# Kernel optimization log

Hardware: AMD Instinct MI355X
Metric: run time of the kernel (lower is better)

## Reference

```python
import jax, jax.numpy as jnp
import numpy as np
import math

B, C, H, W = 8, 64, 64, 64

def setup_inputs() -> dict:
    key = jax.random.key(0)
    k1, k2 = jax.random.split(key)
    x1 = jax.random.normal(k1, (B, C, H, W), dtype=jnp.float32)
    x2 = jax.random.normal(k2, (B, C, H, W), dtype=jnp.float32)
    return {"x1": x1, "x2": x2}

def reference(x1, x2):
    b, c, h, w = x1.shape
    # flatten spatial dims -> tokens: [B, HW, C]
    x1f = x1.reshape(b, c, h * w).transpose(0, 2, 1)
    x2f = x2.reshape(b, c, h * w).transpose(0, 2, 1)
    scale = 1.0 / math.sqrt(c)
    # direction A: queries from x1, keys/values from x2
    scores_a = jnp.einsum('bqc,bkc->bqk', x1f, x2f) * scale  # [B, HW, HW]
    out_a = jnp.einsum('bqk,bkc->bqc', jax.nn.softmax(scores_a, axis=-1), x2f)
    # direction B: queries from x2, keys/values from x1
    scores_b = jnp.einsum('bqc,bkc->bqk', x2f, x1f) * scale
    out_b = jnp.einsum('bqk,bkc->bqc', jax.nn.softmax(scores_b, axis=-1), x1f)
    out = (out_a + out_b).transpose(0, 2, 1).reshape(b, c, h, w)
    return out
```

## Files before the change

kernel.cpp:

```cpp
#include <hip/hip_runtime.h>
#include <hip/hip_bf16.h>
#include <stdint.h>


#define TT 4096
#define CC 64
#define NB 8

typedef float f32x4 __attribute__((ext_vector_type(4)));
typedef float f32x4a __attribute__((ext_vector_type(4), may_alias));
typedef short s16x8 __attribute__((ext_vector_type(8)));
typedef unsigned int u32x2a __attribute__((ext_vector_type(2), may_alias));
typedef unsigned int u32x4a __attribute__((ext_vector_type(4), may_alias));
typedef float f32a __attribute__((may_alias));

static __device__ __forceinline__ unsigned fbits(float x) { return __float_as_uint(x); }
static __device__ __forceinline__ ushort bf16of(float v) {
    return (ushort)((fbits(v) + 0x8000u) >> 16);
}
static __device__ __forceinline__ unsigned pack2(float a, float b) {
    return __builtin_amdgcn_perm(fbits(b) + 0x8000u, fbits(a) + 0x8000u, 0x07060302u);
}
static __device__ __forceinline__ s16x8 load_frag(const void* p) {
    u32x4a t = *(const u32x4a*)p;
    return __builtin_bit_cast(s16x8, t);
}

#define SQC1 0.4246609177f

__global__ void prep_k(const float* __restrict__ x1, const float* __restrict__ x2,
                       ushort* __restrict__ kt, ushort* __restrict__ vt) {
    const int inp = blockIdx.z, b = blockIdx.y, tt = blockIdx.x;
    const float* src = (inp == 0 ? x1 : x2) + (size_t)b * CC * TT;
    const size_t plane = (size_t)TT * CC;
    ushort* kd = kt + (size_t)(inp * NB + b) * plane;
    ushort* vd = vt + (size_t)(inp * NB + b) * plane;
    __shared__ ushort lds[64][72];
    const int tid = threadIdx.x;
    const int c  = tid >> 2;
    const int tg = tid & 3;
    const float* srow = src + (size_t)c * TT + tt * 64 + tg * 16;
    unsigned hw[8];
#pragma unroll
    for (int i = 0; i < 4; ++i) {
        f32x4a v = *(const f32x4a*)(srow + i * 4);
        hw[2 * i]     = pack2(v[0], v[1]);
        hw[2 * i + 1] = pack2(v[2], v[3]);
#pragma unroll
        for (int k = 0; k < 4; ++k) lds[tg * 16 + i * 4 + k][c] = bf16of(v[k] * SQC1);
    }
    {
        ushort* vchunk = vd + (((size_t)tt * 2 + (tg >> 1)) * 4 + (c >> 4)) * 512;
        const int l16v = c & 15;
        const int q0v  = (tg & 1) * 2;
        u32x4a w0 = {hw[0], hw[1], hw[2], hw[3]};
        u32x4a w1 = {hw[4], hw[5], hw[6], hw[7]};
        *(u32x4a*)(vchunk + (size_t)(q0v * 16 + l16v) * 8)       = w0;
        *(u32x4a*)(vchunk + (size_t)((q0v + 1) * 16 + l16v) * 8) = w1;
    }
    __syncthreads();
    const int mt   = tid >> 6;
    const int quad = (tid >> 4) & 3;
    const int l16  = tid & 15;
    const int t    = mt * 16 + l16;
#pragma unroll
    for (int ch = 0; ch < 2; ++ch) {
        u32x4a w = *(const u32x4a*)&lds[t][ch * 32 + quad * 8];
        *(u32x4a*)(kd + (((size_t)tt * 4 + mt) * 2 + ch) * 512 +
                   (size_t)(quad * 16 + l16) * 8) = w;
    }
}

__global__ __attribute__((amdgpu_flat_work_group_size(512, 512)))
void attn_fused_k(const ushort* __restrict__ kt, const ushort* __restrict__ vt,
                  float* __restrict__ out) {
    const int b    = blockIdx.x & 7;
    const int qt   = blockIdx.x >> 3;
    const int tid  = threadIdx.x;
    const int wave = tid >> 6;
    const int lane = tid & 63;
    const int quad = lane >> 4;
    const int l16  = lane & 15;
    const int dir  = wave & 1;
    const int pair = (wave >> 1) & 1;
    const int ks   = wave >> 2;
    const int q0   = qt * 64 + pair * 32;

    const size_t plane = (size_t)TT * CC;
    const ushort* Qp = kt + (size_t)((dir == 0 ? 0 : NB) + b) * plane + (size_t)lane * 8;
    const ushort* Kp = kt + (size_t)((dir == 0 ? NB : 0) + b) * plane + (size_t)lane * 8;
    const ushort* Vp = vt + (size_t)((dir == 0 ? NB : 0) + b) * plane + (size_t)lane * 8;

    __shared__ __align__(16) ushort pbuf[8][2][2][16][72];
    __shared__ float lpx[8][2][16];
    f32a* xbuf = (f32a*)&pbuf[0][0][0][0][0];

    s16x8 qf[2][2];
#pragma unroll
    for (int rb = 0; rb < 2; ++rb)
#pragma unroll
        for (int ch = 0; ch < 2; ++ch)
            qf[rb][ch] = load_frag(Qp + (((size_t)qt * 4 + pair * 2 + rb) * 2 + ch) * 512);

    f32x4 accO[2][4];
#pragma unroll
    for (int rb = 0; rb < 2; ++rb)
#pragma unroll
        for (int ct = 0; ct < 4; ++ct) accO[rb][ct] = (f32x4){0.f, 0.f, 0.f, 0.f};
    float lp[2] = {0.f, 0.f};

    s16x8 kA0, kA1, kA2, kA3, kA4, kA5, kA6, kA7;
    s16x8 kB0, kB1, kB2, kB3, kB4, kB5, kB6, kB7;
    s16x8 vA0, vA1, vA2, vA3, vA4, vA5, vA6, vA7;
    s16x8 vB0, vB1, vB2, vB3, vB4, vB5, vB6, vB7;

    auto loadKA = [&](int j) {
        const ushort* p = Kp + (size_t)(ks * 32 + j) * 4096;
        kA0 = load_frag(p);          kA1 = load_frag(p + 512);
        kA2 = load_frag(p + 1024);   kA3 = load_frag(p + 1536);
        kA4 = load_frag(p + 2048);   kA5 = load_frag(p + 2560);
        kA6 = load_frag(p + 3072);   kA7 = load_frag(p + 3584);
    };
    auto loadKB = [&](int j) {
        const ushort* p = Kp + (size_t)(ks * 32 + j) * 4096;
        kB0 = load_frag(p);          kB1 = load_frag(p + 512);
        kB2 = load_frag(p + 1024);   kB3 = load_frag(p + 1536);
        kB4 = load_frag(p + 2048);   kB5 = load_frag(p + 2560);
        kB6 = load_frag(p + 3072);   kB7 = load_frag(p + 3584);
    };
    auto loadVA = [&](int j) {
        const ushort* p = Vp + (size_t)(ks * 32 + j) * 4096;
        vA0 = load_frag(p);          vA1 = load_frag(p + 512);
        vA2 = load_frag(p + 1024);   vA3 = load_frag(p + 1536);
        vA4 = load_frag(p + 2048);   vA5 = load_frag(p + 2560);
        vA6 = load_frag(p + 3072);   vA7 = load_frag(p + 3584);
    };
    auto loadVB = [&](int j) {
        const ushort* p = Vp + (size_t)(ks * 32 + j) * 4096;
        vB0 = load_frag(p);          vB1 = load_frag(p + 512);
        vB2 = load_frag(p + 1024);   vB3 = load_frag(p + 1536);
        vB4 = load_frag(p + 2048);   vB5 = load_frag(p + 2560);
        vB6 = load_frag(p + 3072);   vB7 = load_frag(p + 3584);
    };

    auto SmT = [&](s16x8 kc0, s16x8 kc1, int mt, int par) {
#pragma unroll
        for (int rb = 0; rb < 2; ++rb) {
            f32x4 s = (f32x4){0.f, 0.f, 0.f, 0.f};
            s = __builtin_amdgcn_mfma_f32_16x16x32_bf16(kc0, qf[rb][0], s, 0, 0, 0);
            s = __builtin_amdgcn_mfma_f32_16x16x32_bf16(kc1, qf[rb][1], s, 0, 0, 0);
            float p0 = __builtin_amdgcn_exp2f(s[0]);
            float p1 = __builtin_amdgcn_exp2f(s[1]);
            float p2 = __builtin_amdgcn_exp2f(s[2]);
            float p3 = __builtin_amdgcn_exp2f(s[3]);
            lp[rb] += (p0 + p1) + (p2 + p3);
            u32x2a w;
            w[0] = pack2(p0, p1);
            w[1] = pack2(p2, p3);
            *(u32x2a*)&pbuf[wave][par][rb][l16][mt * 16 + quad * 4] = w;
        }
    };
    auto PVA = [&]() {
        s16x8 pf0a = load_frag(&pbuf[wave][0][0][l16][quad * 8]);
        s16x8 pf1a = load_frag(&pbuf[wave][0][1][l16][quad * 8]);
        accO[0][0] = __builtin_amdgcn_mfma_f32_16x16x32_bf16(vA0, pf0a, accO[0][0], 0, 0, 0);
        accO[1][0] = __builtin_amdgcn_mfma_f32_16x16x32_bf16(vA0, pf1a, accO[1][0], 0, 0, 0);
        accO[0][1] = __builtin_amdgcn_mfma_f32_16x16x32_bf16(vA1, pf0a, accO[0][1], 0, 0, 0);
        accO[1][1] = __builtin_amdgcn_mfma_f32_16x16x32_bf16(vA1, pf1a, accO[1][1], 0, 0, 0);
        accO[0][2] = __builtin_amdgcn_mfma_f32_16x16x32_bf16(vA2, pf0a, accO[0][2], 0, 0, 0);
        accO[1][2] = __builtin_amdgcn_mfma_f32_16x16x32_bf16(vA2, pf1a, accO[1][2], 0, 0, 0);
        accO[0][3] = __builtin_amdgcn_mfma_f32_16x16x32_bf16(vA3, pf0a, accO[0][3], 0, 0, 0);
        accO[1][3] = __builtin_amdgcn_mfma_f32_16x16x32_bf16(vA3, pf1a, accO[1][3], 0, 0, 0);
        s16x8 pf0b = load_frag(&pbuf[wave][0][0][l16][32 + quad * 8]);
        s16x8 pf1b = load_frag(&pbuf[wave][0][1][l16][32 + quad * 8]);
        accO[0][0] = __builtin_amdgcn_mfma_f32_16x16x32_bf16(vA4, pf0b, accO[0][0], 0, 0, 0);
        accO[1][0] = __builtin_amdgcn_mfma_f32_16x16x32_bf16(vA4, pf1b, accO[1][0], 0, 0, 0);
        accO[0][1] = __builtin_amdgcn_mfma_f32_16x16x32_bf16(vA5, pf0b, accO[0][1], 0, 0, 0);
        accO[1][1] = __builtin_amdgcn_mfma_f32_16x16x32_bf16(vA5, pf1b, accO[1][1], 0, 0, 0);
        accO[0][2] = __builtin_amdgcn_mfma_f32_16x16x32_bf16(vA6, pf0b, accO[0][2], 0, 0, 0);
        accO[1][2] = __builtin_amdgcn_mfma_f32_16x16x32_bf16(vA6, pf1b, accO[1][2], 0, 0, 0);
        accO[0][3] = __builtin_amdgcn_mfma_f32_16x16x32_bf16(vA7, pf0b, accO[0][3], 0, 0, 0);
        accO[1][3] = __builtin_amdgcn_mfma_f32_16x16x32_bf16(vA7, pf1b, accO[1][3], 0, 0, 0);
    };
    auto PVB = [&]() {
        s16x8 pf0a = load_frag(&pbuf[wave][1][0][l16][quad * 8]);
        s16x8 pf1a = load_frag(&pbuf[wave][1][1][l16][quad * 8]);
        accO[0][0] = __builtin_amdgcn_mfma_f32_16x16x32_bf16(vB0, pf0a, accO[0][0], 0, 0, 0);
        accO[1][0] = __builtin_amdgcn_mfma_f32_16x16x32_bf16(vB0, pf1a, accO[1][0], 0, 0, 0);
        accO[0][1] = __builtin_amdgcn_mfma_f32_16x16x32_bf16(vB1, pf0a, accO[0][1], 0, 0, 0);
        accO[1][1] = __builtin_amdgcn_mfma_f32_16x16x32_bf16(vB1, pf1a, accO[1][1], 0, 0, 0);
        accO[0][2] = __builtin_amdgcn_mfma_f32_16x16x32_bf16(vB2, pf0a, accO[0][2], 0, 0, 0);
        accO[1][2] = __builtin_amdgcn_mfma_f32_16x16x32_bf16(vB2, pf1a, accO[1][2], 0, 0, 0);
        accO[0][3] = __builtin_amdgcn_mfma_f32_16x16x32_bf16(vB3, pf0a, accO[0][3], 0, 0, 0);
        accO[1][3] = __builtin_amdgcn_mfma_f32_16x16x32_bf16(vB3, pf1a, accO[1][3], 0, 0, 0);
        s16x8 pf0b = load_frag(&pbuf[wave][1][0][l16][32 + quad * 8]);
        s16x8 pf1b = load_frag(&pbuf[wave][1][1][l16][32 + quad * 8]);
        accO[0][0] = __builtin_amdgcn_mfma_f32_16x16x32_bf16(vB4, pf0b, accO[0][0], 0, 0, 0);
        accO[1][0] = __builtin_amdgcn_mfma_f32_16x16x32_bf16(vB4, pf1b, accO[1][0], 0, 0, 0);
        accO[0][1] = __builtin_amdgcn_mfma_f32_16x16x32_bf16(vB5, pf0b, accO[0][1], 0, 0, 0);
        accO[1][1] = __builtin_amdgcn_mfma_f32_16x16x32_bf16(vB5, pf1b, accO[1][1], 0, 0, 0);
        accO[0][2] = __builtin_amdgcn_mfma_f32_16x16x32_bf16(vB6, pf0b, accO[0][2], 0, 0, 0);
        accO[1][2] = __builtin_amdgcn_mfma_f32_16x16x32_bf16(vB6, pf1b, accO[1][2], 0, 0, 0);
        accO[0][3] = __builtin_amdgcn_mfma_f32_16x16x32_bf16(vB7, pf0b, accO[0][3], 0, 0, 0);
        accO[1][3] = __builtin_amdgcn_mfma_f32_16x16x32_bf16(vB7, pf1b, accO[1][3], 0, 0, 0);
    };

    loadKA(0);
    loadVA(0);
#pragma unroll 1
    for (int j = 0; j < 32; j += 2) {
        loadKB(j + 1);
        SmT(kA0, kA1, 0, 0); SmT(kA2, kA3, 1, 0); SmT(kA4, kA5, 2, 0); SmT(kA6, kA7, 3, 0);
        loadVB(j + 1);
        SmT(kB0, kB1, 0, 1); SmT(kB2, kB3, 1, 1); SmT(kB4, kB5, 2, 1); SmT(kB6, kB7, 3, 1);
        if (j + 2 < 32) loadKA(j + 2);
        PVA();
        if (j + 2 < 32) loadVA(j + 2);
        PVB();
    }

    float inv[2];
#pragma unroll
    for (int rb = 0; rb < 2; ++rb) {
        float l = lp[rb];
        l += __shfl_xor(l, 16);
        l += __shfl_xor(l, 32);
        lp[rb] = l;
        if (lane < 16) lpx[wave][rb][l16] = l;
    }
    __syncthreads();
#pragma unroll
    for (int rb = 0; rb < 2; ++rb)
        inv[rb] = __builtin_amdgcn_rcpf(lp[rb] + lpx[wave ^ 4][rb][l16]);

    const int g = (ks << 1) | dir;
#pragma unroll 1
    for (int ph = 3; ph >= 1; --ph) {
        if (g == ph) {
#pragma unroll
            for (int rb = 0; rb < 2; ++rb)
#pragma unroll
                for (int ct = 0; ct < 4; ++ct)
#pragma unroll
                    for (int r = 0; r < 4; ++r) {
                        const int slot = (pair * 32 + rb * 16 + ct * 4 + r) * 64 + lane;
                        float v = accO[rb][ct][r] * inv[rb];
                        if (ph == 3) xbuf[slot] = v;
                        else xbuf[slot] += v;
                    }
        }
        __syncthreads();
    }
    if (g == 0) {
        float* ob = out + (size_t)b * plane;
#pragma unroll
        for (int rb = 0; rb < 2; ++rb)
#pragma unroll
            for (int ct = 0; ct < 4; ++ct)
#pragma unroll
                for (int r = 0; r < 4; ++r) {
                    float v = accO[rb][ct][r] * inv[rb] +
                              xbuf[(pair * 32 + rb * 16 + ct * 4 + r) * 64 + lane];
                    ob[(size_t)(ct * 16 + quad * 4 + r) * TT + q0 + rb * 16 + l16] = v;
                }
    }
}

extern "C" void kernel_launch(void* const* d_in, const int* in_sizes, int n_in,
                              void* d_out, int out_size, void* d_ws, size_t ws_size,
                              hipStream_t stream) {
    const float* x1 = (const float*)d_in[0];
    const float* x2 = (const float*)d_in[1];
    ushort* kt = (ushort*)d_ws;
    ushort* vt = (ushort*)d_ws + (size_t)2 * NB * TT * CC;

    hipLaunchKernelGGL(prep_k, dim3(TT / 64, NB, 2), dim3(256), 0, stream, x1, x2, kt, vt);
    hipLaunchKernelGGL(attn_fused_k, dim3(64 * NB), dim3(512), 0, stream,
                       kt, vt, (float*)d_out);
}
```

Before: 163.6 us.

## Use 1024-thread blocks covering two query tiles with single-buffered K/V fragments

The attention kernel now runs 16 waves per block, with each block handling two 64-query tiles, so the grid is halved and the shared pbuf/lpx arrays are doubled. The separate A/B register buffers for K and V fragments are merged into one set. The main loop is re-pipelined so the PV step for one parity overlaps with the score step and loads for the other. The goal is to cut register pressure enough to fit 1024-thread blocks and raise the number of resident waves. In exchange there is less register-level prefetch depth, more LDS per block, and a tighter per-wave register budget that could cause spills.

```diff
diff --git a/kernel.cpp b/kernel.cpp
--- a/kernel.cpp
+++ b/kernel.cpp
@@ -71,28 +71,30 @@
     }
 }
 
-__global__ __attribute__((amdgpu_flat_work_group_size(512, 512)))
+__global__ __attribute__((amdgpu_flat_work_group_size(1024, 1024)))
 void attn_fused_k(const ushort* __restrict__ kt, const ushort* __restrict__ vt,
                   float* __restrict__ out) {
-    const int b    = blockIdx.x & 7;
-    const int qt   = blockIdx.x >> 3;
-    const int tid  = threadIdx.x;
-    const int wave = tid >> 6;
-    const int lane = tid & 63;
-    const int quad = lane >> 4;
-    const int l16  = lane & 15;
-    const int dir  = wave & 1;
-    const int pair = (wave >> 1) & 1;
-    const int ks   = wave >> 2;
-    const int q0   = qt * 64 + pair * 32;
+    const int b     = blockIdx.x & 7;
+    const int qt2   = blockIdx.x >> 3;
+    const int tid   = threadIdx.x;
+    const int wave  = tid >> 6;
+    const int lane  = tid & 63;
+    const int quad  = lane >> 4;
+    const int l16   = lane & 15;
+    const int dir   = wave & 1;
+    const int pair  = (wave >> 1) & 1;
+    const int ks    = (wave >> 2) & 1;
+    const int qsub  = wave >> 3;
+    const int qt    = qt2 * 2 + qsub;
+    const int q0    = qt * 64 + pair * 32;
 
     const size_t plane = (size_t)TT * CC;
     const ushort* Qp = kt + (size_t)((dir == 0 ? 0 : NB) + b) * plane + (size_t)lane * 8;
     const ushort* Kp = kt + (size_t)((dir == 0 ? NB : 0) + b) * plane + (size_t)lane * 8;
     const ushort* Vp = vt + (size_t)((dir == 0 ? NB : 0) + b) * plane + (size_t)lane * 8;
 
-    __shared__ __align__(16) ushort pbuf[8][2][2][16][72];
-    __shared__ float lpx[8][2][16];
+    __shared__ __align__(16) ushort pbuf[16][2][2][16][72];
+    __shared__ float lpx[16][2][16];
     f32a* xbuf = (f32a*)&pbuf[0][0][0][0][0];
 
     s16x8 qf[2][2];
@@ -110,40 +112,29 @@
     float lp[2] = {0.f, 0.f};
 
     s16x8 kA0, kA1, kA2, kA3, kA4, kA5, kA6, kA7;
-    s16x8 kB0, kB1, kB2, kB3, kB4, kB5, kB6, kB7;
     s16x8 vA0, vA1, vA2, vA3, vA4, vA5, vA6, vA7;
-    s16x8 vB0, vB1, vB2, vB3, vB4, vB5, vB6, vB7;
-
-    auto loadKA = [&](int j) {
+
+    auto loadK = [&](int j) {
         const ushort* p = Kp + (size_t)(ks * 32 + j) * 4096;
         kA0 = load_frag(p);          kA1 = load_frag(p + 512);
         kA2 = load_frag(p + 1024);   kA3 = load_frag(p + 1536);
         kA4 = load_frag(p + 2048);   kA5 = load_frag(p + 2560);
         kA6 = load_frag(p + 3072);   kA7 = load_frag(p + 3584);
     };
-    auto loadKB = [&](int j) {
-        const ushort* p = Kp + (size_t)(ks * 32 + j) * 4096;
-        kB0 = load_frag(p);          kB1 = load_frag(p + 512);
-        kB2 = load_frag(p + 1024);   kB3 = load_frag(p + 1536);
-        kB4 = load_frag(p + 2048);   kB5 = load_frag(p + 2560);
-        kB6 = load_frag(p + 3072);   kB7 = load_frag(p + 3584);
-    };
-    auto loadVA = [&](int j) {
+    auto loadV = [&](int j) {
         const ushort* p = Vp + (size_t)(ks * 32 + j) * 4096;
         vA0 = load_frag(p);          vA1 = load_frag(p + 512);
         vA2 = load_frag(p + 1024);   vA3 = load_frag(p + 1536);
         vA4 = load_frag(p + 2048);   vA5 = load_frag(p + 2560);
         vA6 = load_frag(p + 3072);   vA7 = load_frag(p + 3584);
     };
-    auto loadVB = [&](int j) {
-        const ushort* p = Vp + (size_t)(ks * 32 + j) * 4096;
-        vB0 = load_frag(p);          vB1 = load_frag(p + 512);
-        vB2 = load_frag(p + 1024);   vB3 = load_frag(p + 1536);
-        vB4 = load_frag(p + 2048);   vB5 = load_frag(p + 2560);
-        vB6 = load_frag(p + 3072);   vB7 = load_frag(p + 3584);
-    };
-
-    auto SmT = [&](s16x8 kc0, s16x8 kc1, int mt, int par) {
+
+    auto SmT = [&](int mt, int par) {
+        s16x8 kc0, kc1;
+        if (mt == 0)      { kc0 = kA0; kc1 = kA1; }
+        else if (mt == 1) { kc0 = kA2; kc1 = kA3; }
+        else if (mt == 2) { kc0 = kA4; kc1 = kA5; }
+        else              { kc0 = kA6; kc1 = kA7; }
 #pragma unroll
         for (int rb = 0; rb < 2; ++rb) {
             f32x4 s = (f32x4){0.f, 0.f, 0.f, 0.f};
@@ -160,9 +151,11 @@
             *(u32x2a*)&pbuf[wave][par][rb][l16][mt * 16 + quad * 4] = w;
         }
     };
-    auto PVA = [&]() {
-        s16x8 pf0a = load_frag(&pbuf[wave][0][0][l16][quad * 8]);
-        s16x8 pf1a = load_frag(&pbuf[wave][0][1][l16][quad * 8]);
+    auto Sphase = [&](int par) { SmT(0, par); SmT(1, par); SmT(2, par); SmT(3, par); };
+
+    auto PVphase = [&](int par) {
+        s16x8 pf0a = load_frag(&pbuf[wave][par][0][l16][quad * 8]);
+        s16x8 pf1a = load_frag(&pbuf[wave][par][1][l16][quad * 8]);
         accO[0][0] = __builtin_amdgcn_mfma_f32_16x16x32_bf16(vA0, pf0a, accO[0][0], 0, 0, 0);
         accO[1][0] = __builtin_amdgcn_mfma_f32_16x16x32_bf16(vA0, pf1a, accO[1][0], 0, 0, 0);
         accO[0][1] = __builtin_amdgcn_mfma_f32_16x16x32_bf16(vA1, pf0a, accO[0][1], 0, 0, 0);
@@ -171,8 +164,8 @@
         accO[1][2] = __builtin_amdgcn_mfma_f32_16x16x32_bf16(vA2, pf1a, accO[1][2], 0, 0, 0);
         accO[0][3] = __builtin_amdgcn_mfma_f32_16x16x32_bf16(vA3, pf0a, accO[0][3], 0, 0, 0);
         accO[1][3] = __builtin_amdgcn_mfma_f32_16x16x32_bf16(vA3, pf1a, accO[1][3], 0, 0, 0);
-        s16x8 pf0b = load_frag(&pbuf[wave][0][0][l16][32 + quad * 8]);
-        s16x8 pf1b = load_frag(&pbuf[wave][0][1][l16][32 + quad * 8]);
+        s16x8 pf0b = load_frag(&pbuf[wave][par][0][l16][32 + quad * 8]);
+        s16x8 pf1b = load_frag(&pbuf[wave][par][1][l16][32 + quad * 8]);
         accO[0][0] = __builtin_amdgcn_mfma_f32_16x16x32_bf16(vA4, pf0b, accO[0][0], 0, 0, 0);
         accO[1][0] = __builtin_amdgcn_mfma_f32_16x16x32_bf16(vA4, pf1b, accO[1][0], 0, 0, 0);
         accO[0][1] = __builtin_amdgcn_mfma_f32_16x16x32_bf16(vA5, pf0b, accO[0][1], 0, 0, 0);
@@ -182,42 +175,20 @@
         accO[0][3] = __builtin_amdgcn_mfma_f32_16x16x32_bf16(vA7, pf0b, accO[0][3], 0, 0, 0);
         accO[1][3] = __builtin_amdgcn_mfma_f32_16x16x32_bf16(vA7, pf1b, accO[1][3], 0, 0, 0);
     };
-    auto PVB = [&]() {
-        s16x8 pf0a = load_frag(&pbuf[wave][1][0][l16][quad * 8]);
-        s16x8 pf1a = load_frag(&pbuf[wave][1][1][l16][quad * 8]);
-        accO[0][0] = __builtin_amdgcn_mfma_f32_16x16x32_bf16(vB0, pf0a, accO[0][0], 0, 0, 0);
-        accO[1][0] = __builtin_amdgcn_mfma_f32_16x16x32_bf16(vB0, pf1a, accO[1][0], 0, 0, 0);
-        accO[0][1] = __builtin_amdgcn_mfma_f32_16x16x32_bf16(vB1, pf0a, accO[0][1], 0, 0, 0);
-        accO[1][1] = __builtin_amdgcn_mfma_f32_16x16x32_bf16(vB1, pf1a, accO[1][1], 0, 0, 0);
-        accO[0][2] = __builtin_amdgcn_mfma_f32_16x16x32_bf16(vB2, pf0a, accO[0][2], 0, 0, 0);
-        accO[1][2] = __builtin_amdgcn_mfma_f32_16x16x32_bf16(vB2, pf1a, accO[1][2], 0, 0, 0);
-        accO[0][3] = __builtin_amdgcn_mfma_f32_16x16x32_bf16(vB3, pf0a, accO[0][3], 0, 0, 0);
-        accO[1][3] = __builtin_amdgcn_mfma_f32_16x16x32_bf16(vB3, pf1a, accO[1][3], 0, 0, 0);
-        s16x8 pf0b = load_frag(&pbuf[wave][1][0][l16][32 + quad * 8]);
-        s16x8 pf1b = load_frag(&pbuf[wave][1][1][l16][32 + quad * 8]);
-        accO[0][0] = __builtin_amdgcn_mfma_f32_16x16x32_bf16(vB4, pf0b, accO[0][0], 0, 0, 0);
-        accO[1][0] = __builtin_amdgcn_mfma_f32_16x16x32_bf16(vB4, pf1b, accO[1][0], 0, 0, 0);
-        accO[0][1] = __builtin_amdgcn_mfma_f32_16x16x32_bf16(vB5, pf0b, accO[0][1], 0, 0, 0);
-        accO[1][1] = __builtin_amdgcn_mfma_f32_16x16x32_bf16(vB5, pf1b, accO[1][1], 0, 0, 0);
-        accO[0][2] = __builtin_amdgcn_mfma_f32_16x16x32_bf16(vB6, pf0b, accO[0][2], 0, 0, 0);
-        accO[1][2] = __builtin_amdgcn_mfma_f32_16x16x32_bf16(vB6, pf1b, accO[1][2], 0, 0, 0);
-        accO[0][3] = __builtin_amdgcn_mfma_f32_16x16x32_bf16(vB7, pf0b, accO[0][3], 0, 0, 0);
-        accO[1][3] = __builtin_amdgcn_mfma_f32_16x16x32_bf16(vB7, pf1b, accO[1][3], 0, 0, 0);
-    };
-
-    loadKA(0);
-    loadVA(0);
+
+    loadK(0);
 #pragma unroll 1
     for (int j = 0; j < 32; j += 2) {
-        loadKB(j + 1);
-        SmT(kA0, kA1, 0, 0); SmT(kA2, kA3, 1, 0); SmT(kA4, kA5, 2, 0); SmT(kA6, kA7, 3, 0);
-        loadVB(j + 1);
-        SmT(kB0, kB1, 0, 1); SmT(kB2, kB3, 1, 1); SmT(kB4, kB5, 2, 1); SmT(kB6, kB7, 3, 1);
-        if (j + 2 < 32) loadKA(j + 2);
-        PVA();
-        if (j + 2 < 32) loadVA(j + 2);
-        PVB();
-    }
+        Sphase(0);
+        loadK(j + 1);
+        if (j > 0) PVphase(1);
+        loadV(j);
+        Sphase(1);
+        if (j + 2 < 32) loadK(j + 2);
+        PVphase(0);
+        loadV(j + 1);
+    }
+    PVphase(1);
 
     float inv[2];
 #pragma unroll
@@ -234,6 +205,7 @@
         inv[rb] = __builtin_amdgcn_rcpf(lp[rb] + lpx[wave ^ 4][rb][l16]);
 
     const int g = (ks << 1) | dir;
+    const int grp = qsub * 2 + pair;
 #pragma unroll 1
     for (int ph = 3; ph >= 1; --ph) {
         if (g == ph) {
@@ -243,7 +215,7 @@
                 for (int ct = 0; ct < 4; ++ct)
 #pragma unroll
                     for (int r = 0; r < 4; ++r) {
-                        const int slot = (pair * 32 + rb * 16 + ct * 4 + r) * 64 + lane;
+                        const int slot = (grp * 32 + rb * 16 + ct * 4 + r) * 64 + lane;
                         float v = accO[rb][ct][r] * inv[rb];
                         if (ph == 3) xbuf[slot] = v;
                         else xbuf[slot] += v;
@@ -260,7 +232,7 @@
 #pragma unroll
                 for (int r = 0; r < 4; ++r) {
                     float v = accO[rb][ct][r] * inv[rb] +
-                              xbuf[(pair * 32 + rb * 16 + ct * 4 + r) * 64 + lane];
+                              xbuf[(grp * 32 + rb * 16 + ct * 4 + r) * 64 + lane];
                     ob[(size_t)(ct * 16 + quad * 4 + r) * TT + q0 + rb * 16 + l16] = v;
                 }
     }
@@ -275,6 +247,6 @@
     ushort* vt = (ushort*)d_ws + (size_t)2 * NB * TT * CC;
 
     hipLaunchKernelGGL(prep_k, dim3(TT / 64, NB, 2), dim3(256), 0, stream, x1, x2, kt, vt);
-    hipLaunchKernelGGL(attn_fused_k, dim3(64 * NB), dim3(512), 0, stream,
+    hipLaunchKernelGGL(attn_fused_k, dim3(32 * NB), dim3(1024), 0, stream,
                        kt, vt, (float*)d_out);
 }
```

After: 599.2 us. +266.2%, slower.
